# Kernel tuning notes

Hardware: AMD Instinct MI355X
Metric: run time of the kernel (lower is better)

## Reference

```python
import jax, jax.numpy as jnp
import numpy as np


def setup_inputs() -> dict:
    key = jax.random.key(0)
    ks = jax.random.split(key, 8)
    B, P, K, N = 8, 16384, 16384, 16
    IN, REL, OUT = 64, 3, 64
    return {
        "keys": jax.random.normal(ks[0], (B, K, REL), dtype=jnp.float32),
        "points": jax.random.normal(ks[1], (B, P, REL), dtype=jnp.float32),
        "feats": jax.random.normal(ks[2], (B, P, IN), dtype=jnp.float32),
        "n_idxs": jax.random.randint(ks[3], (B, K, N), 0, P, dtype=jnp.int32),
        "neighbor_rel": jax.random.normal(ks[4], (B, K, N, REL), dtype=jnp.float32),
        "neighbor_valid": jax.random.randint(ks[5], (B, K, N), 0, 2, dtype=jnp.int32),
        "W": jax.random.normal(ks[6], (OUT, IN + REL), dtype=jnp.float32) / np.sqrt(IN + REL),
        "b": jax.random.normal(ks[7], (OUT,), dtype=jnp.float32) * 0.01,
    }


def reference(keys, points, feats, n_idxs, neighbor_rel, neighbor_valid, W, b):
    # gather neighbor features: feats[b, n_idxs[b]] per batch -> [B, K, N, IN]
    neighbor_feats = jax.vmap(lambda f, i: f[i])(feats, n_idxs)
    comb = jnp.concatenate([neighbor_feats, neighbor_rel], axis=-1)  # [B,K,N,IN+REL]
    valid = neighbor_valid.astype(comb.dtype)                        # [B,K,N]
    cleared = comb * valid[..., None]
    counts = valid.sum(-1)                                           # [B,K]
    inv_counts = jnp.where(counts > 0, 1.0 / jnp.maximum(counts, 1.0), 0.0)
    sum_feats = cleared.sum(axis=2)                                  # [B,K,IN+REL]
    scaled = sum_feats * inv_counts[..., None]
    return jax.nn.relu(jnp.einsum('bkc,oc->bko', scaled, W) + b)
```

## Files before the change

### kernel.cpp

```cpp
#include <hip/hip_runtime.h>

#define BB   8
#define PP   16384
#define KK   16384
#define NN   16
#define CIN  64
#define REL  3
#define CC   67
#define OUTC 64
#define PITCH_US 104


typedef short s16x8 __attribute__((ext_vector_type(8)));
typedef float f32x4 __attribute__((ext_vector_type(4)));
typedef unsigned int u32x2 __attribute__((ext_vector_type(2)));

static __device__ __forceinline__ unsigned short bf16_rne(float f) {
    unsigned int u = __float_as_uint(f);
    u += 0x7FFF + ((u >> 16) & 1);
    return (unsigned short)(u >> 16);
}

template <int PAT>
static __device__ __forceinline__ float swz_add(float v) {
    return v + __int_as_float(
        __builtin_amdgcn_ds_swizzle(__float_as_int(v), PAT));
}

__global__ __launch_bounds__(256, 4) void graphconv_kernel(
    const float* __restrict__ feats,
    const int*   __restrict__ n_idxs,
    const float* __restrict__ neighbor_rel,
    const int*   __restrict__ neighbor_valid,
    const float* __restrict__ Wm,
    const float* __restrict__ bvec,
    float*       __restrict__ out)
{
    __shared__ __align__(16) unsigned short Wbf[OUTC * PITCH_US];
    __shared__ __align__(16) unsigned short Stile[4 * 16 * PITCH_US];

    const int tid = threadIdx.x;

    {
        unsigned int* w32 = (unsigned int*)Wbf;
        for (int j = tid; j < OUTC * (PITCH_US / 2); j += 256) {
            const int o = j / (PITCH_US / 2);
            const int d = j - o * (PITCH_US / 2);
            const int c0 = 2 * d, c1 = 2 * d + 1;
            const float w0 = (c0 < CC) ? Wm[o * CC + c0] : 0.0f;
            const float w1 = (c1 < CC) ? Wm[o * CC + c1] : 0.0f;
            w32[j] = (unsigned int)bf16_rne(w0) |
                     ((unsigned int)bf16_rne(w1) << 16);
        }
    }
    __syncthreads();

    const int lane = tid & 63;
    const int wave = __builtin_amdgcn_readfirstlane(tid >> 6);
    unsigned short* Sw = &Stile[wave * 16 * PITCH_US];

    {
        unsigned int* s32 = (unsigned int*)Sw;
        for (int j = lane; j < 16 * (PITCH_US / 2); j += 64) s32[j] = 0u;
    }

    const int b   = blockIdx.x & 7;
    const int bib = blockIdx.x >> 3;
    const float* fb = feats + (size_t)b * ((size_t)PP * CIN);

    const int q     = lane & 15;
    const int permb = (lane & 48) << 2;

    const int kw = (bib * 4 + wave) * 32;

    for (int g = 0; g < 2; ++g) {
        const int kg = kw + g * 16;
        const size_t rg = (size_t)b * KK + (size_t)kg;

        int   vld[4], idd[4];
        float rl0[4], rl1[4], rl2[4];
#pragma unroll
        for (int qd = 0; qd < 4; ++qd) {
            const size_t rq = rg + (size_t)(qd * 4);
            vld[qd] = neighbor_valid[rq * NN + lane];
            idd[qd] = n_idxs[rq * NN + lane];
            const float* relq = neighbor_rel + rq * (NN * REL);
            rl0[qd] = relq[3 * lane + 0];
            rl1[qd] = relq[3 * lane + 1];
            rl2[qd] = relq[3 * lane + 2];
        }

        for (int qd = 0; qd < 4; ++qd) {
            const int   cmb = idd[qd] | (vld[qd] << 14);
            const float msf = (float)vld[qd];
            float mr0 = msf * rl0[qd];
            float mr1 = msf * rl1[qd];
            float mr2 = msf * rl2[qd];
            float cnt = msf;

            int cm[NN];
#pragma unroll
            for (int n = 0; n < NN; ++n)
                cm[n] = __builtin_amdgcn_ds_bpermute(permb + 4 * n, cmb);

            float s0 = 0.f, s1 = 0.f, s2 = 0.f, s3 = 0.f;
            float4 gv[8];
#pragma unroll
            for (int h = 0; h < 2; ++h) {
#pragma unroll
                for (int n = 0; n < 8; ++n) {
                    const int off = ((cm[h * 8 + n] & 0x3FFF) << 6) + 4 * q;
                    gv[n] = *(const float4*)(fb + off);
                }
                __builtin_amdgcn_sched_barrier(0);
#pragma unroll
                for (int n = 0; n < 8; ++n) {
                    const float m = (float)(cm[h * 8 + n] >> 14);
                    s0 = fmaf(m, gv[n].x, s0);
                    s1 = fmaf(m, gv[n].y, s1);
                    s2 = fmaf(m, gv[n].z, s2);
                    s3 = fmaf(m, gv[n].w, s3);
                }
            }

            cnt = swz_add<0x041F>(cnt); mr0 = swz_add<0x041F>(mr0);
            mr1 = swz_add<0x041F>(mr1); mr2 = swz_add<0x041F>(mr2);
            cnt = swz_add<0x081F>(cnt); mr0 = swz_add<0x081F>(mr0);
            mr1 = swz_add<0x081F>(mr1); mr2 = swz_add<0x081F>(mr2);
            cnt = swz_add<0x101F>(cnt); mr0 = swz_add<0x101F>(mr0);
            mr1 = swz_add<0x101F>(mr1); mr2 = swz_add<0x101F>(mr2);
            cnt = swz_add<0x201F>(cnt); mr0 = swz_add<0x201F>(mr0);
            mr1 = swz_add<0x201F>(mr1); mr2 = swz_add<0x201F>(mr2);

            const float inv = (cnt > 0.f) ? (1.0f / cnt) : 0.0f;

            const int rowl = qd * 4 + (lane >> 4);
            u32x2 pv;
            pv.x = (unsigned)bf16_rne(s0 * inv) |
                   ((unsigned)bf16_rne(s1 * inv) << 16);
            pv.y = (unsigned)bf16_rne(s2 * inv) |
                   ((unsigned)bf16_rne(s3 * inv) << 16);
            *(u32x2*)(&Sw[rowl * PITCH_US + 4 * q]) = pv;
            if (q == 0) {
                u32x2 ev;
                ev.x = (unsigned)bf16_rne(mr0 * inv) |
                       ((unsigned)bf16_rne(mr1 * inv) << 16);
                ev.y = (unsigned)bf16_rne(mr2 * inv);
                *(u32x2*)(&Sw[rowl * PITCH_US + 64]) = ev;
            }
        }

        f32x4 C0 = {0.f,0.f,0.f,0.f}, C1 = {0.f,0.f,0.f,0.f};
        f32x4 C2 = {0.f,0.f,0.f,0.f}, C3 = {0.f,0.f,0.f,0.f};
#pragma unroll
        for (int p = 0; p < 3; ++p) {
            const int ko = p * 32 + (lane >> 4) * 8;
            const s16x8 A  = *(const s16x8*)&Sw[(lane & 15) * PITCH_US + ko];
            const s16x8 B0 = *(const s16x8*)&Wbf[( 0 + (lane & 15)) * PITCH_US + ko];
            const s16x8 B1 = *(const s16x8*)&Wbf[(16 + (lane & 15)) * PITCH_US + ko];
            const s16x8 B2 = *(const s16x8*)&Wbf[(32 + (lane & 15)) * PITCH_US + ko];
            const s16x8 B3 = *(const s16x8*)&Wbf[(48 + (lane & 15)) * PITCH_US + ko];
            C0 = __builtin_amdgcn_mfma_f32_16x16x32_bf16(A, B0, C0, 0, 0, 0);
            C1 = __builtin_amdgcn_mfma_f32_16x16x32_bf16(A, B1, C1, 0, 0, 0);
            C2 = __builtin_amdgcn_mfma_f32_16x16x32_bf16(A, B2, C2, 0, 0, 0);
            C3 = __builtin_amdgcn_mfma_f32_16x16x32_bf16(A, B3, C3, 0, 0, 0);
        }

        const float bias0 = bvec[ 0 + (lane & 15)];
        const float bias1 = bvec[16 + (lane & 15)];
        const float bias2 = bvec[32 + (lane & 15)];
        const float bias3 = bvec[48 + (lane & 15)];
        const int m0 = (lane >> 4) * 4;
        const int oc = lane & 15;
#pragma unroll
        for (int r = 0; r < 4; ++r) {
            const size_t orow = ((size_t)b * KK + (size_t)(kg + m0 + r)) * OUTC;
            out[orow + 0  + oc] = fmaxf(C0[r] + bias0, 0.0f);
            out[orow + 16 + oc] = fmaxf(C1[r] + bias1, 0.0f);
            out[orow + 32 + oc] = fmaxf(C2[r] + bias2, 0.0f);
            out[orow + 48 + oc] = fmaxf(C3[r] + bias3, 0.0f);
        }
    }
}

extern "C" void kernel_launch(void* const* d_in, const int* in_sizes, int n_in,
                              void* d_out, int out_size, void* d_ws, size_t ws_size,
                              hipStream_t stream) {
    const float* feats = (const float*)d_in[2];
    const int*   nidx  = (const int*)  d_in[3];
    const float* nrel  = (const float*)d_in[4];
    const int*   nval  = (const int*)  d_in[5];
    const float* Wm    = (const float*)d_in[6];
    const float* bv    = (const float*)d_in[7];
    float* out = (float*)d_out;

    graphconv_kernel<<<dim3(1024), dim3(256), 0, stream>>>(
        feats, nidx, nrel, nval, Wm, bv, out);
}
```

Measured before the change: 157.1 us.

## Pre-convert feats to bf16 in a workspace pass and gather bf16 rows

Adds a pre-pass kernel that converts the whole feats tensor to bf16 in the workspace, so the main kernel's random neighbor gathers load half as many bytes per row. The gather loop also issues all 16 neighbor loads before a single scheduling barrier instead of two batches of 8, which raises memory-level parallelism at the cost of more live registers. The extra kernel reads 32 MB and writes 16 MB every call, and rounding features to bf16 before summation adds precision loss.

```diff
diff --git a/kernel.cpp b/kernel.cpp
--- a/kernel.cpp
+++ b/kernel.cpp
@@ -27,8 +27,19 @@
         __builtin_amdgcn_ds_swizzle(__float_as_int(v), PAT));
 }
 
+__global__ __launch_bounds__(256) void feats_to_bf16_kernel(
+    const float* __restrict__ f, unsigned short* __restrict__ o)
+{
+    const int i = blockIdx.x * 256 + threadIdx.x;
+    const float4 v = ((const float4*)f)[i];
+    ushort4 r;
+    r.x = bf16_rne(v.x); r.y = bf16_rne(v.y);
+    r.z = bf16_rne(v.z); r.w = bf16_rne(v.w);
+    ((ushort4*)o)[i] = r;
+}
+
 __global__ __launch_bounds__(256, 4) void graphconv_kernel(
-    const float* __restrict__ feats,
+    const unsigned short* __restrict__ fbf16,
     const int*   __restrict__ n_idxs,
     const float* __restrict__ neighbor_rel,
     const int*   __restrict__ neighbor_valid,
@@ -66,7 +77,7 @@
 
     const int b   = blockIdx.x & 7;
     const int bib = blockIdx.x >> 3;
-    const float* fb = feats + (size_t)b * ((size_t)PP * CIN);
+    const unsigned short* fb = fbf16 + (size_t)b * ((size_t)PP * CIN);
 
     const int q     = lane & 15;
     const int permb = (lane & 48) << 2;
@@ -103,24 +114,23 @@
             for (int n = 0; n < NN; ++n)
                 cm[n] = __builtin_amdgcn_ds_bpermute(permb + 4 * n, cmb);
 
+            u32x2 gv[NN];
+#pragma unroll
+            for (int n = 0; n < NN; ++n) {
+                const int off = ((cm[n] & 0x3FFF) << 6) + 4 * q;
+                gv[n] = *(const u32x2*)(fb + off);
+            }
+            __builtin_amdgcn_sched_barrier(0);
+
             float s0 = 0.f, s1 = 0.f, s2 = 0.f, s3 = 0.f;
-            float4 gv[8];
-#pragma unroll
-            for (int h = 0; h < 2; ++h) {
-#pragma unroll
-                for (int n = 0; n < 8; ++n) {
-                    const int off = ((cm[h * 8 + n] & 0x3FFF) << 6) + 4 * q;
-                    gv[n] = *(const float4*)(fb + off);
-                }
-                __builtin_amdgcn_sched_barrier(0);
-#pragma unroll
-                for (int n = 0; n < 8; ++n) {
-                    const float m = (float)(cm[h * 8 + n] >> 14);
-                    s0 = fmaf(m, gv[n].x, s0);
-                    s1 = fmaf(m, gv[n].y, s1);
-                    s2 = fmaf(m, gv[n].z, s2);
-                    s3 = fmaf(m, gv[n].w, s3);
-                }
+#pragma unroll
+            for (int n = 0; n < NN; ++n) {
+                const float m = (float)(cm[n] >> 14);
+                const unsigned ux = gv[n].x, uy = gv[n].y;
+                s0 = fmaf(m, __uint_as_float(ux << 16), s0);
+                s1 = fmaf(m, __uint_as_float(ux & 0xFFFF0000u), s1);
+                s2 = fmaf(m, __uint_as_float(uy << 16), s2);
+                s3 = fmaf(m, __uint_as_float(uy & 0xFFFF0000u), s3);
             }
 
             cnt = swz_add<0x041F>(cnt); mr0 = swz_add<0x041F>(mr0);
@@ -194,6 +204,10 @@
     const float* bv    = (const float*)d_in[7];
     float* out = (float*)d_out;
 
+    unsigned short* fbf16 = (unsigned short*)d_ws;
+
+    feats_to_bf16_kernel<<<dim3(8192), dim3(256), 0, stream>>>(feats, fbf16);
+
     graphconv_kernel<<<dim3(1024), dim3(256), 0, stream>>>(
-        feats, nidx, nrel, nval, Wm, bv, out);
-}
+        fbf16, nidx, nrel, nval, Wm, bv, out);
+}
```

Result: no change. 155.6 us (-0.9%).
